# Optimization experiments

Hardware: AMD Instinct MI355X
Metric: run time of the kernel (lower is better)

The kernel has to match this reference:

```python
import jax, jax.numpy as jnp
import numpy as np

R_FRAC = 0.5  # r_token


def setup_inputs() -> dict:
    key = jax.random.key(0)
    B, T, C = 64, 577, 1024
    hidden_states = jax.random.normal(key, (B, T, C), dtype=jnp.float32)
    return {"hidden_states": hidden_states}


def _match_indices(x, r):
    # Bipartite soft matching (class_token=True, distill_token=False).
    metric = x / jnp.linalg.norm(x, axis=-1, keepdims=True)
    a, b = metric[:, ::2, :], metric[:, 1::2, :]  # [B, Ta, C], [B, Tb, C]
    scores = jnp.einsum('bic,bjc->bij', a, b)     # [B, Ta, Tb]
    scores = scores.at[:, 0, :].set(-jnp.inf)     # protect CLS token (even index 0)
    node_max = scores.max(axis=-1)                # best sim of each src to any dst
    node_idx = scores.argmax(axis=-1)             # matched dst for each src
    edge_idx = jnp.argsort(-node_max, axis=-1)    # descending by similarity
    unm_idx = jnp.sort(edge_idx[:, r:], axis=-1)  # unmerged src (sorted: keeps CLS first)
    src_idx = edge_idx[:, :r]                     # src tokens to merge
    dst_idx = jnp.take_along_axis(node_idx, src_idx, axis=-1)
    return unm_idx, src_idx, dst_idx


def _merge_sum(v, unm_idx, src_idx, dst_idx):
    # Gather unmerged + scatter-add merged src into dst, then concat.
    src, dst = v[:, ::2, :], v[:, 1::2, :]
    unm = jnp.take_along_axis(src, unm_idx[..., None], axis=1)
    srcg = jnp.take_along_axis(src, src_idx[..., None], axis=1)
    dst = jax.vmap(lambda d, i, s: d.at[i].add(s))(dst, dst_idx, srcg)
    return jnp.concatenate([unm, dst], axis=1)


def reference(hidden_states):
    x = hidden_states
    B, T, C = x.shape
    protected = 1  # class token
    r = min(int(R_FRAC * T), (T - protected) // 2)  # 288 for T=577
    unm_idx, src_idx, dst_idx = _match_indices(x, r)
    # merge_wavg with size=None -> size = ones
    size = jnp.ones((B, T, 1), dtype=x.dtype)
    xm = _merge_sum(x * size, unm_idx, src_idx, dst_idx)
    sm = _merge_sum(size, unm_idx, src_idx, dst_idx)
    return xm / sm  # [B, T - r, C]
```

## Files before the change

### kernel.cpp

```cpp
#include <hip/hip_runtime.h>
#include <math.h>


#define B_   64
#define T_   577
#define C_   1024
#define NA   289
#define NB   288
#define EPS_MARGIN 0.04f

#define RPAD 384
#define EXTRA_CAP 12

typedef __bf16 bf16x8 __attribute__((ext_vector_type(8)));
typedef float  floatx4 __attribute__((ext_vector_type(4)));
typedef unsigned long long u64;

#define ECNT_OFF   0
#define GRPWIN_OFF 98304
#define EXTRA_OFF  (GRPWIN_OFF + 1179648)
#define DST_OFF    (EXTRA_OFF + 2359296)

__device__ __forceinline__ u64 shfl_xor_u64(u64 v, int msk) {
  unsigned int lo = (unsigned int)v, hi = (unsigned int)(v >> 32);
  lo = __shfl_xor(lo, msk, 64);
  hi = __shfl_xor(hi, msk, 64);
  return ((u64)hi << 32) | (u64)lo;
}
__device__ __forceinline__ double shfl_xor_f64(double v, int msk) {
  u64 u = __double_as_longlong(v);
  return __longlong_as_double((long long)shfl_xor_u64(u, msk));
}

__device__ __forceinline__ unsigned int fkey(float s) {
  unsigned int fb = __float_as_uint(s);
  return (fb & 0x80000000u) ? ~fb : (fb | 0x80000000u);
}
__device__ __forceinline__ float keyf(unsigned int k) {
  return (k & 0x80000000u) ? __uint_as_float(k ^ 0x80000000u) : __uint_as_float(~k);
}
__device__ __forceinline__ u64 packsc(float s, int col) {
  return ((u64)fkey(s) << 32) | (u64)(0xFFFFFFFFu - (unsigned int)col);
}
__device__ __forceinline__ int pcol(u64 p) {
  return (int)(0xFFFFFFFFu - (unsigned int)(p & 0xFFFFFFFFull));
}
__device__ __forceinline__ float pscore(u64 p) { return keyf((unsigned int)(p >> 32)); }

__device__ __forceinline__ unsigned int pk_bf16_trunc(unsigned int e1, unsigned int e0) {
  return __builtin_amdgcn_perm(e1, e0, 0x07060302u);
}

__device__ __forceinline__ void load16f(const float* x, size_t off, float* v) {
  const float4* p = (const float4*)(x + off);
  float4 a = p[0], b = p[1], c = p[2], d = p[3];
  v[0]=a.x; v[1]=a.y; v[2]=a.z; v[3]=a.w;
  v[4]=b.x; v[5]=b.y; v[6]=b.z; v[7]=b.w;
  v[8]=c.x; v[9]=c.y; v[10]=c.z; v[11]=c.w;
  v[12]=d.x; v[13]=d.y; v[14]=d.z; v[15]=d.w;
}

__global__ __launch_bounds__(256, 2) void k_scores(const float* __restrict__ x,
                                                   u64* __restrict__ grpwin,
                                                   unsigned int* __restrict__ ecnt,
                                                   u64* __restrict__ extras) {
  __shared__ unsigned char smem[2][24576];
  __shared__ float sumsq[96];
  int tid = threadIdx.x;
  int b  = blockIdx.x;
  int rt = blockIdx.y;
  int ct = blockIdx.z;
  int wv = tid >> 6, lane = tid & 63;
  int m = lane & 15, q = lane >> 4;
  int sw = m & 7;

  if (tid < 96) sumsq[tid] = 0.f;

  const float* eptr[6];
  int eoff[6];
#pragma unroll
  for (int e = 0; e < 6; ++e) {
    int v = tid + 256 * e;
    int isB = v >= 768;
    int w = isB ? v - 768 : v;
    int row = w >> 3, slot = w & 7;
    int gk = slot ^ (row & 7);
    int tok;
    if (isB) tok = 2 * (ct * 96 + row) + 1;
    else { tok = 2 * (rt * 96 + row); if (tok > 576) tok = 576; }
    eptr[e] = x + (size_t)(b * T_ + tok) * C_ + gk * 8;
    eoff[e] = (isB ? 12288 : 0) + row * 128 + slot * 16;
  }

  float ssp[3] = {0.f, 0.f, 0.f};
  uint4 L[6][2];

#pragma unroll
  for (int e = 0; e < 6; ++e) {
    const uint4* p = (const uint4*)(eptr[e]);
    L[e][0] = p[0]; L[e][1] = p[1];
  }
#pragma unroll
  for (int e = 0; e < 6; ++e) {
    uint4 lo = L[e][0], hi = L[e][1];
    uint4 o;
    o.x = pk_bf16_trunc(lo.y, lo.x);
    o.y = pk_bf16_trunc(lo.w, lo.z);
    o.z = pk_bf16_trunc(hi.y, hi.x);
    o.w = pk_bf16_trunc(hi.w, hi.z);
    *(uint4*)(smem[0] + eoff[e]) = o;
    if (e >= 3) {
      float f0 = __uint_as_float(lo.x), f1 = __uint_as_float(lo.y);
      float f2 = __uint_as_float(lo.z), f3 = __uint_as_float(lo.w);
      float f4 = __uint_as_float(hi.x), f5 = __uint_as_float(hi.y);
      float f6 = __uint_as_float(hi.z), f7 = __uint_as_float(hi.w);
      ssp[e-3] += f0*f0 + f1*f1 + f2*f2 + f3*f3 + f4*f4 + f5*f5 + f6*f6 + f7*f7;
    }
  }
  __syncthreads();

  floatx4 acc[3][3];
#pragma unroll
  for (int ii = 0; ii < 3; ++ii)
#pragma unroll
    for (int jj = 0; jj < 3; ++jj) acc[ii][jj] = (floatx4){0,0,0,0};

  const int ib = (wv >> 1) * 3;
  const int jb = (wv & 1) * 3;

  for (int kc = 0; kc < 16; ++kc) {
    const unsigned char* buf = smem[kc & 1];
    unsigned char* nbuf = smem[(kc + 1) & 1];
    if (kc < 15) {
#pragma unroll
      for (int e = 0; e < 6; ++e) {
        const uint4* p = (const uint4*)(eptr[e] + (kc + 1) * 64);
        L[e][0] = p[0]; L[e][1] = p[1];
      }
    }
#pragma unroll
    for (int s = 0; s < 2; ++s) {
      int slot = (s * 4 + q) ^ sw;
      bf16x8 af[3], bf[3];
#pragma unroll
      for (int ii = 0; ii < 3; ++ii)
        af[ii] = *(const bf16x8*)(buf + ((ib + ii) * 16 + m) * 128 + slot * 16);
#pragma unroll
      for (int jj = 0; jj < 3; ++jj)
        bf[jj] = *(const bf16x8*)(buf + 12288 + ((jb + jj) * 16 + m) * 128 + slot * 16);
#pragma unroll
      for (int ii = 0; ii < 3; ++ii)
#pragma unroll
        for (int jj = 0; jj < 3; ++jj)
          acc[ii][jj] = __builtin_amdgcn_mfma_f32_16x16x32_bf16(af[ii], bf[jj], acc[ii][jj], 0,0,0);
    }
    if (kc < 15) {
#pragma unroll
      for (int e = 0; e < 6; ++e) {
        uint4 lo = L[e][0], hi = L[e][1];
        uint4 o;
        o.x = pk_bf16_trunc(lo.y, lo.x);
        o.y = pk_bf16_trunc(lo.w, lo.z);
        o.z = pk_bf16_trunc(hi.y, hi.x);
        o.w = pk_bf16_trunc(hi.w, hi.z);
        *(uint4*)(nbuf + eoff[e]) = o;
        if (e >= 3) {
          float f0 = __uint_as_float(lo.x), f1 = __uint_as_float(lo.y);
          float f2 = __uint_as_float(lo.z), f3 = __uint_as_float(lo.w);
          float f4 = __uint_as_float(hi.x), f5 = __uint_as_float(hi.y);
          float f6 = __uint_as_float(hi.z), f7 = __uint_as_float(hi.w);
          ssp[e-3] += f0*f0 + f1*f1 + f2*f2 + f3*f3 + f4*f4 + f5*f5 + f6*f6 + f7*f7;
        }
      }
    }
    __syncthreads();
  }

#pragma unroll
  for (int e = 3; e < 6; ++e) {
    int w = tid + 256 * e - 768;
    atomicAdd(&sumsq[w >> 3], ssp[e-3]);
  }
  __syncthreads();

  float rn[3];
#pragma unroll
  for (int jj = 0; jj < 3; ++jj) rn[jj] = rsqrtf(sumsq[(jb + jj) * 16 + m]);

  int g = ct * 2 + (wv & 1);
#pragma unroll
  for (int ii = 0; ii < 3; ++ii) {
#pragma unroll
    for (int r = 0; r < 4; ++r) {
      u64 pj[3];
#pragma unroll
      for (int jj = 0; jj < 3; ++jj) {
        float s = acc[ii][jj][r] * rn[jj];
        pj[jj] = packsc(s, ct * 96 + (jb + jj) * 16 + m);
      }
      u64 pk = pj[0];
      if (pj[1] > pk) pk = pj[1];
      if (pj[2] > pk) pk = pj[2];
#pragma unroll
      for (int d = 1; d < 16; d <<= 1) {
        u64 o = shfl_xor_u64(pk, d);
        if (o > pk) pk = o;
      }
      int grow = rt * 96 + (ib + ii) * 16 + q * 4 + r;
      float thr = pscore(pk) - EPS_MARGIN;
      size_t rbase = (size_t)b * RPAD + grow;
#pragma unroll
      for (int jj = 0; jj < 3; ++jj) {
        if (pj[jj] != pk && pscore(pj[jj]) >= thr) {
          unsigned int idx = atomicAdd(&ecnt[rbase], 1u);
          if (idx < EXTRA_CAP) extras[rbase * EXTRA_CAP + idx] = pj[jj];
        }
      }
      if (m == 0) grpwin[rbase * 6 + g] = pk;
    }
  }
}

__global__ __launch_bounds__(256) void k_recheck(const float* __restrict__ x,
                                                 const u64* __restrict__ grpwin,
                                                 const unsigned int* __restrict__ ecnt,
                                                 const u64* __restrict__ extras,
                                                 int* __restrict__ dst) {
  int wid = threadIdx.x >> 6, lane = threadIdx.x & 63;
  int gw = blockIdx.x * 4 + wid;
  int b = gw / NB, i = gw - b * NB + 1;
  size_t rbase = (size_t)b * RPAD + i;

  u64 v = (lane < 6) ? grpwin[rbase * 6 + lane] : 0ull;
#pragma unroll
  for (int d = 1; d < 8; d <<= 1) {
    u64 o = shfl_xor_u64(v, d);
    if (o > v) v = o;
  }
  {
    unsigned int lo = (unsigned int)v, hi = (unsigned int)(v >> 32);
    lo = __shfl(lo, 0, 64); hi = __shfl(hi, 0, 64);
    v = ((u64)hi << 32) | lo;
  }
  float thr = pscore(v) - EPS_MARGIN;

  u64 cand[14]; int nc = 0;
#pragma unroll
  for (int t = 0; t < 6; ++t) {
    u64 w = grpwin[rbase * 6 + t];
    if (pscore(w) >= thr && nc < 14) cand[nc++] = w;
  }
  unsigned int ec = ecnt[rbase]; if (ec > EXTRA_CAP) ec = EXTRA_CAP;
  for (unsigned int t = 0; t < ec; ++t) {
    u64 w = extras[rbase * EXTRA_CAP + t];
    if (pscore(w) >= thr && nc < 14) cand[nc++] = w;
  }

  int best;
  if (nc <= 1) {
    best = pcol(v);
  } else {
    float av[16];
    load16f(x, (size_t)(b * T_ + 2 * i) * C_ + lane * 16, av);
    double bs = -1e300; int bc = 1 << 30;
    for (int c = 0; c < nc; ++c) {
      int col = pcol(cand[c]);
      float bv[16];
      load16f(x, (size_t)(b * T_ + 2 * col + 1) * C_ + lane * 16, bv);
      double dot = 0.0, nsq = 0.0;
#pragma unroll
      for (int t = 0; t < 16; ++t) {
        dot += (double)av[t] * (double)bv[t];
        nsq += (double)bv[t] * (double)bv[t];
      }
#pragma unroll
      for (int d = 32; d >= 1; d >>= 1) {
        dot += shfl_xor_f64(dot, d);
        nsq += shfl_xor_f64(nsq, d);
      }
      double s = dot / sqrt(nsq);
      if (s > bs || (s == bs && col < bc)) { bs = s; bc = col; }
    }
    best = bc;
  }
  if (lane == 0) dst[b * NA + i] = best;
}

__global__ __launch_bounds__(256) void k_merge(const float* __restrict__ x,
                                               const int* __restrict__ dst,
                                               float* __restrict__ out) {
  __shared__ int dstv[NA];
  __shared__ unsigned short lists[4][292];
  __shared__ int cnts[4];
  int b = blockIdx.y, tid = threadIdx.x;
  int orow_base = blockIdx.x * 4;

  for (int i = tid; i < NA; i += 256) dstv[i] = (i >= 1) ? dst[b * NA + i] : -1;
  if (tid < 4) cnts[tid] = 0;
  __syncthreads();

  for (int i = 1 + tid; i <= 288; i += 256) {
    int d = dstv[i];
#pragma unroll
    for (int w4 = 0; w4 < 4; ++w4) {
      int orow_w = orow_base + w4;
      if (orow_w >= 1 && orow_w < NA && d == orow_w - 1) {
        int idx = atomicAdd(&cnts[w4], 1);
        lists[w4][idx] = (unsigned short)i;
      }
    }
  }
  __syncthreads();

  int wv = tid >> 6, lane = tid & 63;
  int orow = orow_base + wv;
  if (orow >= NA) return;

  const size_t xb = (size_t)b * T_ * C_;
  int c0 = lane * 16;
  float acc[16];
  float inv = 1.0f;

  if (orow == 0) {
    load16f(x, xb + c0, acc);
  } else {
    int j = orow - 1;
    load16f(x, xb + (size_t)(2 * j + 1) * C_ + c0, acc);
    int cnt = cnts[wv];
    for (int e = 0; e < cnt; ++e) {
      int i = lists[wv][e];
      float tv[16];
      load16f(x, xb + (size_t)(2 * i) * C_ + c0, tv);
#pragma unroll
      for (int t = 0; t < 16; ++t) acc[t] += tv[t];
    }
    inv = 1.0f / (float)(cnt + 1);
  }

  float4* op = (float4*)(out + ((size_t)b * NA + orow) * C_ + c0);
  op[0] = make_float4(acc[0]*inv,  acc[1]*inv,  acc[2]*inv,  acc[3]*inv);
  op[1] = make_float4(acc[4]*inv,  acc[5]*inv,  acc[6]*inv,  acc[7]*inv);
  op[2] = make_float4(acc[8]*inv,  acc[9]*inv,  acc[10]*inv, acc[11]*inv);
  op[3] = make_float4(acc[12]*inv, acc[13]*inv, acc[14]*inv, acc[15]*inv);
}

extern "C" void kernel_launch(void* const* d_in, const int* in_sizes, int n_in,
                              void* d_out, int out_size, void* d_ws, size_t ws_size,
                              hipStream_t stream) {
  const float* x = (const float*)d_in[0];
  float* out     = (float*)d_out;
  char* ws = (char*)d_ws;
  unsigned int* ecnt = (unsigned int*)(ws + ECNT_OFF);
  u64* grpwin        = (u64*)(ws + GRPWIN_OFF);
  u64* extras        = (u64*)(ws + EXTRA_OFF);
  int* dst           = (int*)(ws + DST_OFF);

  hipMemsetAsync(ecnt, 0, (size_t)B_ * RPAD * sizeof(unsigned int), stream);
  k_scores <<<dim3(B_, 4, 3), 256, 0, stream>>>(x, grpwin, ecnt, extras);
  k_recheck<<<B_ * NB / 4, 256, 0, stream>>>(x, grpwin, ecnt, extras, dst);
  k_merge  <<<dim3((NA + 3) / 4, B_), 256, 0, stream>>>(x, dst, out);
}
```

Measured before the change: 309.1 us.

## Prefetch two K-chunks ahead in score GEMM and tighten bf16 rescoring margin

```diff
diff --git a/kernel.cpp b/kernel.cpp
--- a/kernel.cpp
+++ b/kernel.cpp
@@ -7,7 +7,7 @@
 #define C_   1024
 #define NA   289
 #define NB   288
-#define EPS_MARGIN 0.04f
+#define EPS_MARGIN 0.01f
 
 #define RPAD 384
 #define EXTRA_CAP 12
@@ -59,6 +59,57 @@
   v[8]=c.x; v[9]=c.y; v[10]=c.z; v[11]=c.w;
   v[12]=d.x; v[13]=d.y; v[14]=d.z; v[15]=d.w;
 }
+
+
+#define LOADC(S, KCC) do {                                                    \
+  _Pragma("unroll")                                                           \
+  for (int e_ = 0; e_ < 6; ++e_) {                                            \
+    const uint4* p_ = (const uint4*)(eptr[e_] + (KCC) * 64);                  \
+    S[e_][0] = p_[0]; S[e_][1] = p_[1];                                       \
+  }                                                                           \
+} while (0)
+
+#define STAGEC(S, BUFP) do {                                                  \
+  unsigned char* sb_ = (BUFP);                                                \
+  _Pragma("unroll")                                                           \
+  for (int e_ = 0; e_ < 6; ++e_) {                                            \
+    uint4 lo_ = S[e_][0], hi_ = S[e_][1];                                     \
+    uint4 o_;                                                                 \
+    o_.x = pk_bf16_trunc(lo_.y, lo_.x);                                       \
+    o_.y = pk_bf16_trunc(lo_.w, lo_.z);                                       \
+    o_.z = pk_bf16_trunc(hi_.y, hi_.x);                                       \
+    o_.w = pk_bf16_trunc(hi_.w, hi_.z);                                       \
+    *(uint4*)(sb_ + eoff[e_]) = o_;                                           \
+    if (e_ >= 3) {                                                            \
+      float f0_ = __uint_as_float(lo_.x), f1_ = __uint_as_float(lo_.y);       \
+      float f2_ = __uint_as_float(lo_.z), f3_ = __uint_as_float(lo_.w);       \
+      float f4_ = __uint_as_float(hi_.x), f5_ = __uint_as_float(hi_.y);       \
+      float f6_ = __uint_as_float(hi_.z), f7_ = __uint_as_float(hi_.w);       \
+      ssp[e_-3] += f0_*f0_ + f1_*f1_ + f2_*f2_ + f3_*f3_                      \
+                 + f4_*f4_ + f5_*f5_ + f6_*f6_ + f7_*f7_;                     \
+    }                                                                         \
+  }                                                                           \
+} while (0)
+
+#define MFMAC(BUFP) do {                                                      \
+  const unsigned char* buf_ = (BUFP);                                         \
+  _Pragma("unroll")                                                           \
+  for (int s_ = 0; s_ < 2; ++s_) {                                            \
+    int slot_ = (s_ * 4 + q) ^ sw;                                            \
+    bf16x8 af_[3], bg_[3];                                                    \
+    _Pragma("unroll")                                                         \
+    for (int ii_ = 0; ii_ < 3; ++ii_)                                         \
+      af_[ii_] = *(const bf16x8*)(buf_ + ((ib + ii_) * 16 + m) * 128 + slot_ * 16); \
+    _Pragma("unroll")                                                         \
+    for (int jj_ = 0; jj_ < 3; ++jj_)                                         \
+      bg_[jj_] = *(const bf16x8*)(buf_ + 12288 + ((jb + jj_) * 16 + m) * 128 + slot_ * 16); \
+    _Pragma("unroll")                                                         \
+    for (int ii_ = 0; ii_ < 3; ++ii_)                                         \
+      _Pragma("unroll")                                                       \
+      for (int jj_ = 0; jj_ < 3; ++jj_)                                       \
+        acc[ii_][jj_] = __builtin_amdgcn_mfma_f32_16x16x32_bf16(af_[ii_], bg_[jj_], acc[ii_][jj_], 0, 0, 0); \
+  }                                                                           \
+} while (0)
 
 __global__ __launch_bounds__(256, 2) void k_scores(const float* __restrict__ x,
                                                    u64* __restrict__ grpwin,
@@ -93,31 +144,7 @@
   }
 
   float ssp[3] = {0.f, 0.f, 0.f};
-  uint4 L[6][2];
-
-#pragma unroll
-  for (int e = 0; e < 6; ++e) {
-    const uint4* p = (const uint4*)(eptr[e]);
-    L[e][0] = p[0]; L[e][1] = p[1];
-  }
-#pragma unroll
-  for (int e = 0; e < 6; ++e) {
-    uint4 lo = L[e][0], hi = L[e][1];
-    uint4 o;
-    o.x = pk_bf16_trunc(lo.y, lo.x);
-    o.y = pk_bf16_trunc(lo.w, lo.z);
-    o.z = pk_bf16_trunc(hi.y, hi.x);
-    o.w = pk_bf16_trunc(hi.w, hi.z);
-    *(uint4*)(smem[0] + eoff[e]) = o;
-    if (e >= 3) {
-      float f0 = __uint_as_float(lo.x), f1 = __uint_as_float(lo.y);
-      float f2 = __uint_as_float(lo.z), f3 = __uint_as_float(lo.w);
-      float f4 = __uint_as_float(hi.x), f5 = __uint_as_float(hi.y);
-      float f6 = __uint_as_float(hi.z), f7 = __uint_as_float(hi.w);
-      ssp[e-3] += f0*f0 + f1*f1 + f2*f2 + f3*f3 + f4*f4 + f5*f5 + f6*f6 + f7*f7;
-    }
-  }
-  __syncthreads();
+  uint4 SA[6][2], SB[6][2];
 
   floatx4 acc[3][3];
 #pragma unroll
@@ -128,53 +155,28 @@
   const int ib = (wv >> 1) * 3;
   const int jb = (wv & 1) * 3;
 
-  for (int kc = 0; kc < 16; ++kc) {
-    const unsigned char* buf = smem[kc & 1];
-    unsigned char* nbuf = smem[(kc + 1) & 1];
-    if (kc < 15) {
-#pragma unroll
-      for (int e = 0; e < 6; ++e) {
-        const uint4* p = (const uint4*)(eptr[e] + (kc + 1) * 64);
-        L[e][0] = p[0]; L[e][1] = p[1];
-      }
-    }
-#pragma unroll
-    for (int s = 0; s < 2; ++s) {
-      int slot = (s * 4 + q) ^ sw;
-      bf16x8 af[3], bf[3];
-#pragma unroll
-      for (int ii = 0; ii < 3; ++ii)
-        af[ii] = *(const bf16x8*)(buf + ((ib + ii) * 16 + m) * 128 + slot * 16);
-#pragma unroll
-      for (int jj = 0; jj < 3; ++jj)
-        bf[jj] = *(const bf16x8*)(buf + 12288 + ((jb + jj) * 16 + m) * 128 + slot * 16);
-#pragma unroll
-      for (int ii = 0; ii < 3; ++ii)
-#pragma unroll
-        for (int jj = 0; jj < 3; ++jj)
-          acc[ii][jj] = __builtin_amdgcn_mfma_f32_16x16x32_bf16(af[ii], bf[jj], acc[ii][jj], 0,0,0);
-    }
-    if (kc < 15) {
-#pragma unroll
-      for (int e = 0; e < 6; ++e) {
-        uint4 lo = L[e][0], hi = L[e][1];
-        uint4 o;
-        o.x = pk_bf16_trunc(lo.y, lo.x);
-        o.y = pk_bf16_trunc(lo.w, lo.z);
-        o.z = pk_bf16_trunc(hi.y, hi.x);
-        o.w = pk_bf16_trunc(hi.w, hi.z);
-        *(uint4*)(nbuf + eoff[e]) = o;
-        if (e >= 3) {
-          float f0 = __uint_as_float(lo.x), f1 = __uint_as_float(lo.y);
-          float f2 = __uint_as_float(lo.z), f3 = __uint_as_float(lo.w);
-          float f4 = __uint_as_float(hi.x), f5 = __uint_as_float(hi.y);
-          float f6 = __uint_as_float(hi.z), f7 = __uint_as_float(hi.w);
-          ssp[e-3] += f0*f0 + f1*f1 + f2*f2 + f3*f3 + f4*f4 + f5*f5 + f6*f6 + f7*f7;
-        }
-      }
-    }
+  LOADC(SA, 0);
+  LOADC(SB, 1);
+  __builtin_amdgcn_sched_barrier(0);
+  STAGEC(SA, smem[0]);
+  __syncthreads();
+
+  for (int kc2 = 0; kc2 < 14; kc2 += 2) {
+    LOADC(SA, kc2 + 2);
+    __builtin_amdgcn_sched_barrier(0);
+    STAGEC(SB, smem[1]);
+    MFMAC(smem[0]);
     __syncthreads();
-  }
+    LOADC(SB, kc2 + 3);
+    __builtin_amdgcn_sched_barrier(0);
+    STAGEC(SA, smem[0]);
+    MFMAC(smem[1]);
+    __syncthreads();
+  }
+  STAGEC(SB, smem[1]);
+  MFMAC(smem[0]);
+  __syncthreads();
+  MFMAC(smem[1]);
 
 #pragma unroll
   for (int e = 3; e < 6; ++e) {
```

New measurement: 319.4 us. 1.03x slower.
